# Kernel tuning notes

Hardware: AMD Instinct MI355X
Metric: run time of the kernel (lower is better)

The kernel has to match this reference:

```python
import jax, jax.numpy as jnp
import numpy as np

N_HEAD = 16
RMS_EPS = 1.1920928955078125e-07  # torch F.rms_norm default eps = finfo(fp32).eps


def _rope_tables(seq_len, head_dim, dtype):
    steps = jnp.arange(seq_len, dtype=jnp.float32)
    rates = 10000.0 ** (-jnp.arange(0, head_dim, 2, dtype=jnp.float32) / head_dim)
    angles = jnp.outer(steps, rates)  # [S, D/2]
    return jnp.cos(angles).astype(dtype)[None, None], jnp.sin(angles).astype(dtype)[None, None]


def _apply_rotary(x, cos, sin):
    # interleaved RoPE: pairs (x[2i], x[2i+1]) rotated
    left = x[..., ::2]
    right = x[..., 1::2]
    lo = left * cos - right * sin
    ro = left * sin + right * cos
    return jnp.stack((lo, ro), axis=-1).reshape(x.shape)


def _rms_norm(x, eps=RMS_EPS):
    ms = jnp.mean(jnp.square(x), axis=-1, keepdims=True)
    return x * jax.lax.rsqrt(ms + eps)


def setup_inputs() -> dict:
    key = jax.random.key(0)
    k1, k2, k3 = jax.random.split(key, 3)
    B, S, E = 2, 2048, 2048
    x = jax.random.normal(k1, (B, S, E), dtype=jnp.float32)
    w_qkv = jax.random.normal(k2, (3 * E, E), dtype=jnp.float32) * (E ** -0.5)
    w_proj = jax.random.normal(k3, (E, E), dtype=jnp.float32) * (E ** -0.5)
    return {"x": x, "w_qkv": w_qkv, "w_proj": w_proj}


def reference(x, w_qkv, w_proj):
    B, S, E = x.shape
    H = N_HEAD
    D = E // H

    qkv = x @ w_qkv.T  # [B, S, 3E]
    q, k, v = jnp.split(qkv, 3, axis=-1)
    # [B, S, E] -> [B, H, S, D]
    q = q.reshape(B, S, H, D).transpose(0, 2, 1, 3)
    k = k.reshape(B, S, H, D).transpose(0, 2, 1, 3)
    v = v.reshape(B, S, H, D).transpose(0, 2, 1, 3)

    cos, sin = _rope_tables(S, D, x.dtype)  # [1,1,S,D/2]
    q = _apply_rotary(q, cos, sin)
    k = _apply_rotary(k, cos, sin)

    q = _rms_norm(q)
    k = _rms_norm(k)

    scale = 1.0 / jnp.sqrt(jnp.asarray(D, dtype=x.dtype))
    scores = jnp.einsum("bhqd,bhkd->bhqk", q, k) * scale  # [B,H,S,S]
    causal = jnp.tril(jnp.ones((S, S), dtype=bool))
    scores = jnp.where(causal[None, None], scores, jnp.asarray(-jnp.inf, dtype=scores.dtype))
    attn = jax.nn.softmax(scores, axis=-1)
    y = jnp.einsum("bhqk,bhkd->bhqd", attn, v)  # [B,H,S,D]
    y = y.transpose(0, 2, 1, 3).reshape(B, S, E)
    return y @ w_proj.T
```

## Files before the change

### kernel.cpp

```cpp
#include <hip/hip_runtime.h>

typedef unsigned short ushort_t;
using bf16x8 = __attribute__((ext_vector_type(8))) short;
using f32x4  = __attribute__((ext_vector_type(4))) float;

#define DEV static __device__ __forceinline__

DEV unsigned short f2bf(float f) {
  union { float f; unsigned u; } a; a.f = f;
  unsigned r = a.u + 0x7fffu + ((a.u >> 16) & 1u);
  return (unsigned short)(r >> 16);
}
DEV float bf2f(unsigned short u) {
  union { unsigned u; float f; } a; a.u = ((unsigned)u) << 16;
  return a.f;
}
DEV void load_lds16(const void* g, void* l) {
  __builtin_amdgcn_global_load_lds(
      (const __attribute__((address_space(1))) void*)g,
      (__attribute__((address_space(3))) void*)l, 16, 0, 0);
}

__global__ __launch_bounds__(256) void cast_kernel(
    const float* __restrict__ src, ushort_t* __restrict__ dst, int n4) {
  int i = blockIdx.x * 256 + threadIdx.x;
  if (i >= n4) return;
  float4 f = ((const float4*)src)[i];
  ushort4 o;
  o.x = f2bf(f.x); o.y = f2bf(f.y); o.z = f2bf(f.z); o.w = f2bf(f.w);
  ((ushort4*)dst)[i] = o;
}

__global__ __launch_bounds__(256) void rope_tables_kernel(float* __restrict__ tab) {
  int idx = blockIdx.x * 256 + threadIdx.x;
  int s = idx >> 6, i = idx & 63;
  float rate = exp2f(-13.287712379549449f * ((float)(2 * i) * (1.0f / 128.0f)));
  float ang = (float)s * rate;
  tab[idx * 2]     = cosf(ang);
  tab[idx * 2 + 1] = sinf(ang);
}

template<int BM, int BN, int OUTF32>
__global__ __launch_bounds__(256, 2) void gemm_bal(
    const ushort_t* __restrict__ A, const ushort_t* __restrict__ Bm,
    void* __restrict__ C, int M, int N, int K) {
  constexpr int MF   = BM / 32;
  constexpr int NF   = BN / 32;
  constexpr int NCA  = BM / 64;
  constexpr int NCB  = BN / 64;
  constexpr int NC   = NCA + NCB;
  constexpr int ABY  = BM * 64;
  constexpr int BUFB = (BM + BN) * 64;
  __shared__ __align__(16) char lds[2 * BUFB];

  const int nby = M / BM;
  const int nwg = nby * (N / BN);
  const int orig = blockIdx.x;
  const int wgid = (orig & 7) * (nwg >> 3) + (orig >> 3);
  const int bm = (wgid % nby) * BM;
  const int bn = (wgid / nby) * BN;

  const int tid = threadIdx.x;
  const int lane = tid & 63;
  const int wave = tid >> 6;
  const int ql = lane & 15, lk = lane >> 4;
  const int wm = wave >> 1, wn = wave & 1;

  f32x4 acc[MF][NF];
#pragma unroll
  for (int m = 0; m < MF; ++m)
#pragma unroll
    for (int n = 0; n < NF; ++n) acc[m][n] = (f32x4){0.f, 0.f, 0.f, 0.f};

  const int rin  = tid >> 2;
  const int sswz = ((tid & 3) ^ ((rin >> 1) & 3)) * 16;
  const size_t rb = (size_t)K * 2;
  const char* src[NC];
#pragma unroll
  for (int c = 0; c < NCA; ++c)
    src[c] = (const char*)A + (size_t)(bm + c * 64 + rin) * rb + sswz;
#pragma unroll
  for (int c = 0; c < NCB; ++c)
    src[NCA + c] = (const char*)Bm + (size_t)(bn + c * 64 + rin) * rb + sswz;
  char* const ldsc = (char*)lds;
  const int dT = tid * 16;

  int aOff[MF], bOff[NF];
#pragma unroll
  for (int m = 0; m < MF; ++m) {
    const int r = wm * (BM / 2) + m * 16 + ql;
    aOff[m] = r * 64 + ((lk ^ ((r >> 1) & 3)) * 16);
  }
#pragma unroll
  for (int n = 0; n < NF; ++n) {
    const int r = wn * (BN / 2) + n * 16 + ql;
    bOff[n] = ABY + r * 64 + ((lk ^ ((r >> 1) & 3)) * 16);
  }

#define STAGE(BB, KT) do {                                   \
    char* d_ = ldsc + (BB) * BUFB + dT;                      \
    const size_t ko_ = (size_t)(KT) * 64;                    \
    _Pragma("unroll")                                        \
    for (int c = 0; c < NC; ++c)                             \
      load_lds16(src[c] + ko_, d_ + c * 4096);               \
  } while (0)
#define MFMA(a, b, c) __builtin_amdgcn_mfma_f32_16x16x32_bf16(a, b, c, 0, 0, 0)

  const int ns = K >> 5;
  STAGE(0, 0);
  __syncthreads();

  for (int t = 0; t < ns; ++t) {
    const int nk = (t + 1 < ns) ? t + 1 : t;
    STAGE((t + 1) & 1, nk);
    const char* sb = ldsc + (t & 1) * BUFB;
    bf16x8 bF[NF], aF[MF];
#pragma unroll
    for (int n = 0; n < NF; ++n) bF[n] = *(const bf16x8*)(sb + bOff[n]);
#pragma unroll
    for (int m = 0; m < MF; ++m) aF[m] = *(const bf16x8*)(sb + aOff[m]);
    __builtin_amdgcn_s_setprio(1);
#pragma unroll
    for (int m = 0; m < MF; ++m)
#pragma unroll
      for (int n = 0; n < NF; ++n)
        acc[m][n] = MFMA(aF[m], bF[n], acc[m][n]);
    __builtin_amdgcn_s_setprio(0);
    __syncthreads();
  }
#undef STAGE
#undef MFMA

#pragma unroll
  for (int m = 0; m < MF; ++m)
#pragma unroll
    for (int i = 0; i < 4; ++i) {
      const size_t row = (size_t)(bm + wm * (BM / 2) + m * 16 + lk * 4 + i);
#pragma unroll
      for (int n = 0; n < NF; ++n) {
        const size_t col = (size_t)(bn + wn * (BN / 2) + n * 16 + ql);
        float v = acc[m][n][i];
        if (OUTF32) ((float*)C)[row * (size_t)N + col] = v;
        else        ((ushort_t*)C)[row * (size_t)N + col] = f2bf(v);
      }
    }
}

__global__ __launch_bounds__(256) void rope_rms_kernel(
    const ushort_t* __restrict__ qkv, ushort_t* __restrict__ q,
    ushort_t* __restrict__ k, ushort_t* __restrict__ vt,
    const float* __restrict__ tab) {
  const int lane = threadIdx.x & 63;
  const int row  = blockIdx.x * 4 + (threadIdx.x >> 6);
  const int h = row & 15;
  int t = row >> 4;
  const int which = t % 3; t /= 3;
  const int s = t & 2047;
  const int b = t >> 11;
  const size_t src = ((size_t)(b * 2048 + s)) * 6144 + which * 2048 + h * 128 + lane * 2;
  ushort2 xv = *(const ushort2*)&qkv[src];
  if (which == 2) {
    size_t vbase = ((size_t)((b * 16 + h) * 128 + lane * 2)) * 2048 + s;
    vt[vbase]        = xv.x;
    vt[vbase + 2048] = xv.y;
    return;
  }
  float lo = bf2f(xv.x), ro = bf2f(xv.y);
  const float2 cs = *(const float2*)&tab[(s * 64 + lane) * 2];
  float l2 = lo * cs.x - ro * cs.y;
  float r2 = lo * cs.y + ro * cs.x;
  float ss = l2 * l2 + r2 * r2;
#pragma unroll
  for (int off = 1; off < 64; off <<= 1) ss += __shfl_xor(ss, off);
  float inv = rsqrtf(ss * (1.0f / 128.0f) + 1.1920928955078125e-07f);
  if (which == 0) inv *= 0.1275174398f;
  lo = l2 * inv; ro = r2 * inv;
  ushort_t* dst = (which == 0) ? q : k;
  ushort2 o; o.x = f2bf(lo); o.y = f2bf(ro);
  *(ushort2*)&dst[(((size_t)(b * 16 + h)) * 2048 + s) * 128 + lane * 2] = o;
}

__global__ __launch_bounds__(256, 1) void attn_kernel(
    const ushort_t* __restrict__ Q, const ushort_t* __restrict__ K,
    const ushort_t* __restrict__ VT, ushort_t* __restrict__ Y) {
  __shared__ __align__(16) ushort_t sK[2][64 * 128];
  __shared__ __align__(16) ushort_t sV[2][128 * 64];
  const int bh = blockIdx.x;
  const int yp = blockIdx.y;
  const int wave = threadIdx.x >> 6, lane = threadIdx.x & 63;
  const int ql = lane & 15, lk = lane >> 4;
  const size_t hq = (size_t)bh * 2048 * 128;
  const int b = bh >> 4, h = bh & 15;

  const char* kB = (const char*)(K + hq);
  const char* vB = (const char*)(VT + hq);
  const char* kSrc[4]; char* kDst[4];
  const char* vSrc[4]; char* vDst[4];
#pragma unroll
  for (int t = 0; t < 4; ++t) {
    int r = wave * 16 + t * 4 + (lane >> 4);
    int kgr = r >> 4, lkr = (r >> 2) & 3, ir = r & 3;
    int rho = (kgr >> 1) * 32 + lkr * 8 + (kgr & 1) * 4 + ir;
    kSrc[t] = kB + rho * 256 + (((lane & 15) * 16) ^ ((r & 7) << 4));
    kDst[t] = (char*)sK + (wave * 256 + t * 64 + lane) * 16;
    int d = wave * 32 + t * 8 + (lane >> 3);
    vSrc[t] = vB + (size_t)d * 4096 + (((lane & 7) * 16) ^ ((d & 7) << 4));
    vDst[t] = (char*)sV + (wave * 256 + t * 64 + lane) * 16;
  }

#define STAGEKV(KT, BB) do {                                         \
    _Pragma("unroll")                                                \
    for (int t_ = 0; t_ < 4; ++t_) {                                 \
      load_lds16(kSrc[t_] + (size_t)(KT) * 16384, kDst[t_] + (BB) * 16384); \
      load_lds16(vSrc[t_] + (KT) * 128, vDst[t_] + (BB) * 16384);    \
    }                                                                \
  } while (0)

  int buf = 0;
  STAGEKV(0, 0);
  __syncthreads();

  for (int pass = 0; pass < 2; ++pass) {
    const int qt = pass ? (15 - yp) : yp;
    const int ktmax = 2 * qt + 1;
    const int q0 = qt * 128 + wave * 32 + ql;

    bf16x8 qf[2][4];
#pragma unroll
    for (int g = 0; g < 2; ++g)
#pragma unroll
      for (int ks = 0; ks < 4; ++ks)
        qf[g][ks] = *(const bf16x8*)&Q[hq + (size_t)(q0 + g * 16) * 128 + ks * 32 + lk * 8];

    f32x4 acc[2][8];
#pragma unroll
    for (int g = 0; g < 2; ++g)
#pragma unroll
      for (int dg = 0; dg < 8; ++dg) acc[g][dg] = (f32x4){0.f, 0.f, 0.f, 0.f};
    float mrow[2] = {-3.0e38f, -3.0e38f}, lsum[2] = {0.f, 0.f};

    for (int kt = 0; kt <= ktmax; ++kt) {
      const int nk = (kt < ktmax) ? kt + 1 : (pass == 0 ? 0 : ktmax);
      STAGEKV(nk, buf ^ 1);
      const char* sKb = (const char*)sK + buf * 16384;
      const char* sVb = (const char*)sV + buf * 16384;

      f32x4 st[2][4];
#pragma unroll
      for (int g = 0; g < 2; ++g)
#pragma unroll
        for (int kg = 0; kg < 4; ++kg) st[g][kg] = (f32x4){0.f, 0.f, 0.f, 0.f};
#pragma unroll
      for (int kg = 0; kg < 4; ++kg) {
        const int row = kg * 16 + ql;
        const int rswz = (row & 7) << 4;
#pragma unroll
        for (int ks = 0; ks < 4; ++ks) {
          bf16x8 kf = *(const bf16x8*)(sKb + row * 256 + ((ks * 64 + lk * 16) ^ rswz));
          st[0][kg] = __builtin_amdgcn_mfma_f32_16x16x32_bf16(kf, qf[0][ks], st[0][kg], 0, 0, 0);
          st[1][kg] = __builtin_amdgcn_mfma_f32_16x16x32_bf16(kf, qf[1][ks], st[1][kg], 0, 0, 0);
        }
      }
      bf16x8 pb[2][2];
#pragma unroll
      for (int g = 0; g < 2; ++g) {
        const int q = q0 + g * 16;
        float sv[4][4]; float mp = -3.0e38f;
#pragma unroll
        for (int kg = 0; kg < 4; ++kg) {
          const int kl = ((kg >> 1) << 5) + lk * 8 + ((kg & 1) << 2);
#pragma unroll
          for (int i = 0; i < 4; ++i) {
            const int key = kt * 64 + kl + i;
            float v = (key <= q) ? st[g][kg][i] : -3.0e38f;
            sv[kg][i] = v;
            mp = fmaxf(mp, v);
          }
        }
        mp = fmaxf(mp, __shfl_xor(mp, 16));
        mp = fmaxf(mp, __shfl_xor(mp, 32));
        const float mn = fmaxf(mrow[g], mp);
        const float corr = exp2f(mrow[g] - mn);
        mrow[g] = mn;
        float p[4][4]; float rs = 0.f;
#pragma unroll
        for (int kg = 0; kg < 4; ++kg)
#pragma unroll
          for (int i = 0; i < 4; ++i) {
            float e = exp2f(sv[kg][i] - mn);
            p[kg][i] = e; rs += e;
          }
        rs += __shfl_xor(rs, 16);
        rs += __shfl_xor(rs, 32);
        lsum[g] = lsum[g] * corr + rs;
#pragma unroll
        for (int dg = 0; dg < 8; ++dg)
#pragma unroll
          for (int i = 0; i < 4; ++i) acc[g][dg][i] *= corr;
#pragma unroll
        for (int c = 0; c < 2; ++c) {
          union { bf16x8 v; ushort_t u[8]; } pk;
#pragma unroll
          for (int j = 0; j < 8; ++j) pk.u[j] = f2bf(p[2 * c + (j >> 2)][j & 3]);
          pb[g][c] = pk.v;
        }
      }
#pragma unroll
      for (int dg = 0; dg < 8; ++dg) {
        const int d = dg * 16 + ql;
        const int dswz = (d & 7) << 4;
#pragma unroll
        for (int c = 0; c < 2; ++c) {
          bf16x8 vf = *(const bf16x8*)(sVb + d * 128 + ((c * 64 + lk * 16) ^ dswz));
          acc[0][dg] = __builtin_amdgcn_mfma_f32_16x16x32_bf16(vf, pb[0][c], acc[0][dg], 0, 0, 0);
          acc[1][dg] = __builtin_amdgcn_mfma_f32_16x16x32_bf16(vf, pb[1][c], acc[1][dg], 0, 0, 0);
        }
      }
      __syncthreads();
      buf ^= 1;
    }

#pragma unroll
    for (int g = 0; g < 2; ++g) {
      const float inv = 1.0f / lsum[g];
      const size_t orow = ((size_t)(b * 2048 + q0 + g * 16)) * 2048 + h * 128;
#pragma unroll
      for (int dg = 0; dg < 8; ++dg) {
        ushort4 o;
        o.x = f2bf(acc[g][dg][0] * inv);
        o.y = f2bf(acc[g][dg][1] * inv);
        o.z = f2bf(acc[g][dg][2] * inv);
        o.w = f2bf(acc[g][dg][3] * inv);
        *(ushort4*)&Y[orow + dg * 16 + lk * 4] = o;
      }
    }
  }
#undef STAGEKV
}

extern "C" void kernel_launch(void* const* d_in, const int* in_sizes, int n_in,
                              void* d_out, int out_size, void* d_ws, size_t ws_size,
                              hipStream_t stream) {
  const float* x     = (const float*)d_in[0];
  const float* wqkv  = (const float*)d_in[1];
  const float* wproj = (const float*)d_in[2];
  float* out = (float*)d_out;
  char* ws = (char*)d_ws;

  ushort_t* x_bf     = (ushort_t*)(ws);
  ushort_t* wqkv_bf  = (ushort_t*)(ws + 16777216);
  ushort_t* wproj_bf = (ushort_t*)(ws + 41943040);
  ushort_t* qkv_bf   = (ushort_t*)(ws + 50331648);
  ushort_t* q_bf     = (ushort_t*)(ws + 100663296);
  ushort_t* k_bf     = (ushort_t*)(ws + 117440512);
  ushort_t* vt_bf    = (ushort_t*)(ws + 134217728);
  float*    tab      = (float*)(ws + 150994944);
  if (ws_size < 152043520u) return;

  cast_kernel<<<8192, 256, 0, stream>>>(x, x_bf, 2097152);
  cast_kernel<<<12288, 256, 0, stream>>>(wqkv, wqkv_bf, 3145728);
  cast_kernel<<<4096, 256, 0, stream>>>(wproj, wproj_bf, 1048576);
  rope_tables_kernel<<<512, 256, 0, stream>>>(tab);

  gemm_bal<256, 128, 0><<<768, 256, 0, stream>>>(x_bf, wqkv_bf, qkv_bf, 4096, 6144, 2048);

  rope_rms_kernel<<<49152, 256, 0, stream>>>(qkv_bf, q_bf, k_bf, vt_bf, tab);

  attn_kernel<<<dim3(32, 8), 256, 0, stream>>>(q_bf, k_bf, vt_bf, qkv_bf );

  gemm_bal<128, 128, 1><<<512, 256, 0, stream>>>(qkv_bf, wproj_bf, out, 4096, 2048, 2048);
}
```

Measured before the change: 339.8 us.

## Split attention into one block per query tile and merge cast kernels

The attention kernel previously paired two query tiles (yp and 15-yp) per block across two sequential passes over 256 blocks. It now launches 512 blocks, each handling a single query tile, ordered heaviest-first so the longer causal tiles start early. Launch bounds change to allow two blocks per CU. The three fp32-to-bf16 cast launches are also fused into one kernel that branches on the index range. This should raise parallelism and occupancy on a 256-CU part and trim launch overhead, at the cost of relying on the hardware scheduler to balance the now-uneven block sizes and possible register pressure under the tighter bound.

```diff
diff --git a/kernel.cpp b/kernel.cpp
--- a/kernel.cpp
+++ b/kernel.cpp
@@ -21,14 +21,19 @@
       (__attribute__((address_space(3))) void*)l, 16, 0, 0);
 }
 
-__global__ __launch_bounds__(256) void cast_kernel(
-    const float* __restrict__ src, ushort_t* __restrict__ dst, int n4) {
+__global__ __launch_bounds__(256) void cast3_kernel(
+    const float* __restrict__ x, const float* __restrict__ wqkv,
+    const float* __restrict__ wproj, ushort_t* __restrict__ xb,
+    ushort_t* __restrict__ qb, ushort_t* __restrict__ pb) {
   int i = blockIdx.x * 256 + threadIdx.x;
-  if (i >= n4) return;
-  float4 f = ((const float4*)src)[i];
+  const float4* s; ushort4* d; int off;
+  if (i < 2097152)      { s = (const float4*)x;     d = (ushort4*)xb; off = i; }
+  else if (i < 5242880) { s = (const float4*)wqkv;  d = (ushort4*)qb; off = i - 2097152; }
+  else                  { s = (const float4*)wproj; d = (ushort4*)pb; off = i - 5242880; }
+  float4 f = s[off];
   ushort4 o;
   o.x = f2bf(f.x); o.y = f2bf(f.y); o.z = f2bf(f.z); o.w = f2bf(f.w);
-  ((ushort4*)dst)[i] = o;
+  d[off] = o;
 }
 
 __global__ __launch_bounds__(256) void rope_tables_kernel(float* __restrict__ tab) {
@@ -180,13 +185,14 @@
   *(ushort2*)&dst[(((size_t)(b * 16 + h)) * 2048 + s) * 128 + lane * 2] = o;
 }
 
-__global__ __launch_bounds__(256, 1) void attn_kernel(
+__global__ __launch_bounds__(256, 2) void attn_kernel(
     const ushort_t* __restrict__ Q, const ushort_t* __restrict__ K,
     const ushort_t* __restrict__ VT, ushort_t* __restrict__ Y) {
   __shared__ __align__(16) ushort_t sK[2][64 * 128];
   __shared__ __align__(16) ushort_t sV[2][128 * 64];
-  const int bh = blockIdx.x;
-  const int yp = blockIdx.y;
+  const int gx = blockIdx.x;
+  const int bh = gx & 31;
+  const int qt = (gx < 256) ? (15 - (gx >> 5)) : ((gx - 256) >> 5);
   const int wave = threadIdx.x >> 6, lane = threadIdx.x & 63;
   const int ql = lane & 15, lk = lane >> 4;
   const size_t hq = (size_t)bh * 2048 * 128;
@@ -216,123 +222,120 @@
     }                                                                \
   } while (0)
 
-  int buf = 0;
+  const int ktmax = 2 * qt + 1;
+  const int q0 = qt * 128 + wave * 32 + ql;
+
+  bf16x8 qf[2][4];
+#pragma unroll
+  for (int g = 0; g < 2; ++g)
+#pragma unroll
+    for (int ks = 0; ks < 4; ++ks)
+      qf[g][ks] = *(const bf16x8*)&Q[hq + (size_t)(q0 + g * 16) * 128 + ks * 32 + lk * 8];
+
+  f32x4 acc[2][8];
+#pragma unroll
+  for (int g = 0; g < 2; ++g)
+#pragma unroll
+    for (int dg = 0; dg < 8; ++dg) acc[g][dg] = (f32x4){0.f, 0.f, 0.f, 0.f};
+  float mrow[2] = {-3.0e38f, -3.0e38f}, lsum[2] = {0.f, 0.f};
+
   STAGEKV(0, 0);
   __syncthreads();
-
-  for (int pass = 0; pass < 2; ++pass) {
-    const int qt = pass ? (15 - yp) : yp;
-    const int ktmax = 2 * qt + 1;
-    const int q0 = qt * 128 + wave * 32 + ql;
-
-    bf16x8 qf[2][4];
+  int buf = 0;
+
+  for (int kt = 0; kt <= ktmax; ++kt) {
+    const int nk = (kt < ktmax) ? kt + 1 : kt;
+    STAGEKV(nk, buf ^ 1);
+    const char* sKb = (const char*)sK + buf * 16384;
+    const char* sVb = (const char*)sV + buf * 16384;
+
+    f32x4 st[2][4];
 #pragma unroll
     for (int g = 0; g < 2; ++g)
 #pragma unroll
-      for (int ks = 0; ks < 4; ++ks)
-        qf[g][ks] = *(const bf16x8*)&Q[hq + (size_t)(q0 + g * 16) * 128 + ks * 32 + lk * 8];
-
-    f32x4 acc[2][8];
-#pragma unroll
-    for (int g = 0; g < 2; ++g)
-#pragma unroll
-      for (int dg = 0; dg < 8; ++dg) acc[g][dg] = (f32x4){0.f, 0.f, 0.f, 0.f};
-    float mrow[2] = {-3.0e38f, -3.0e38f}, lsum[2] = {0.f, 0.f};
-
-    for (int kt = 0; kt <= ktmax; ++kt) {
-      const int nk = (kt < ktmax) ? kt + 1 : (pass == 0 ? 0 : ktmax);
-      STAGEKV(nk, buf ^ 1);
-      const char* sKb = (const char*)sK + buf * 16384;
-      const char* sVb = (const char*)sV + buf * 16384;
-
-      f32x4 st[2][4];
-#pragma unroll
-      for (int g = 0; g < 2; ++g)
-#pragma unroll
-        for (int kg = 0; kg < 4; ++kg) st[g][kg] = (f32x4){0.f, 0.f, 0.f, 0.f};
+      for (int kg = 0; kg < 4; ++kg) st[g][kg] = (f32x4){0.f, 0.f, 0.f, 0.f};
+#pragma unroll
+    for (int kg = 0; kg < 4; ++kg) {
+      const int row = kg * 16 + ql;
+      const int rswz = (row & 7) << 4;
+#pragma unroll
+      for (int ks = 0; ks < 4; ++ks) {
+        bf16x8 kf = *(const bf16x8*)(sKb + row * 256 + ((ks * 64 + lk * 16) ^ rswz));
+        st[0][kg] = __builtin_amdgcn_mfma_f32_16x16x32_bf16(kf, qf[0][ks], st[0][kg], 0, 0, 0);
+        st[1][kg] = __builtin_amdgcn_mfma_f32_16x16x32_bf16(kf, qf[1][ks], st[1][kg], 0, 0, 0);
+      }
+    }
+    bf16x8 pb[2][2];
+#pragma unroll
+    for (int g = 0; g < 2; ++g) {
+      const int q = q0 + g * 16;
+      float sv[4][4]; float mp = -3.0e38f;
 #pragma unroll
       for (int kg = 0; kg < 4; ++kg) {
-        const int row = kg * 16 + ql;
-        const int rswz = (row & 7) << 4;
-#pragma unroll
-        for (int ks = 0; ks < 4; ++ks) {
-          bf16x8 kf = *(const bf16x8*)(sKb + row * 256 + ((ks * 64 + lk * 16) ^ rswz));
-          st[0][kg] = __builtin_amdgcn_mfma_f32_16x16x32_bf16(kf, qf[0][ks], st[0][kg], 0, 0, 0);
-          st[1][kg] = __builtin_amdgcn_mfma_f32_16x16x32_bf16(kf, qf[1][ks], st[1][kg], 0, 0, 0);
+        const int kl = ((kg >> 1) << 5) + lk * 8 + ((kg & 1) << 2);
+#pragma unroll
+        for (int i = 0; i < 4; ++i) {
+          const int key = kt * 64 + kl + i;
+          float v = (key <= q) ? st[g][kg][i] : -3.0e38f;
+          sv[kg][i] = v;
+          mp = fmaxf(mp, v);
         }
       }
-      bf16x8 pb[2][2];
-#pragma unroll
-      for (int g = 0; g < 2; ++g) {
-        const int q = q0 + g * 16;
-        float sv[4][4]; float mp = -3.0e38f;
-#pragma unroll
-        for (int kg = 0; kg < 4; ++kg) {
-          const int kl = ((kg >> 1) << 5) + lk * 8 + ((kg & 1) << 2);
-#pragma unroll
-          for (int i = 0; i < 4; ++i) {
-            const int key = kt * 64 + kl + i;
-            float v = (key <= q) ? st[g][kg][i] : -3.0e38f;
-            sv[kg][i] = v;
-            mp = fmaxf(mp, v);
-          }
+      mp = fmaxf(mp, __shfl_xor(mp, 16));
+      mp = fmaxf(mp, __shfl_xor(mp, 32));
+      const float mn = fmaxf(mrow[g], mp);
+      const float corr = exp2f(mrow[g] - mn);
+      mrow[g] = mn;
+      float p[4][4]; float rs = 0.f;
+#pragma unroll
+      for (int kg = 0; kg < 4; ++kg)
+#pragma unroll
+        for (int i = 0; i < 4; ++i) {
+          float e = exp2f(sv[kg][i] - mn);
+          p[kg][i] = e; rs += e;
         }
-        mp = fmaxf(mp, __shfl_xor(mp, 16));
-        mp = fmaxf(mp, __shfl_xor(mp, 32));
-        const float mn = fmaxf(mrow[g], mp);
-        const float corr = exp2f(mrow[g] - mn);
-        mrow[g] = mn;
-        float p[4][4]; float rs = 0.f;
-#pragma unroll
-        for (int kg = 0; kg < 4; ++kg)
-#pragma unroll
-          for (int i = 0; i < 4; ++i) {
-            float e = exp2f(sv[kg][i] - mn);
-            p[kg][i] = e; rs += e;
-          }
-        rs += __shfl_xor(rs, 16);
-        rs += __shfl_xor(rs, 32);
-        lsum[g] = lsum[g] * corr + rs;
-#pragma unroll
-        for (int dg = 0; dg < 8; ++dg)
-#pragma unroll
-          for (int i = 0; i < 4; ++i) acc[g][dg][i] *= corr;
-#pragma unroll
-        for (int c = 0; c < 2; ++c) {
-          union { bf16x8 v; ushort_t u[8]; } pk;
-#pragma unroll
-          for (int j = 0; j < 8; ++j) pk.u[j] = f2bf(p[2 * c + (j >> 2)][j & 3]);
-          pb[g][c] = pk.v;
-        }
-      }
-#pragma unroll
-      for (int dg = 0; dg < 8; ++dg) {
-        const int d = dg * 16 + ql;
-        const int dswz = (d & 7) << 4;
-#pragma unroll
-        for (int c = 0; c < 2; ++c) {
-          bf16x8 vf = *(const bf16x8*)(sVb + d * 128 + ((c * 64 + lk * 16) ^ dswz));
-          acc[0][dg] = __builtin_amdgcn_mfma_f32_16x16x32_bf16(vf, pb[0][c], acc[0][dg], 0, 0, 0);
-          acc[1][dg] = __builtin_amdgcn_mfma_f32_16x16x32_bf16(vf, pb[1][c], acc[1][dg], 0, 0, 0);
-        }
-      }
-      __syncthreads();
-      buf ^= 1;
-    }
-
-#pragma unroll
-    for (int g = 0; g < 2; ++g) {
-      const float inv = 1.0f / lsum[g];
-      const size_t orow = ((size_t)(b * 2048 + q0 + g * 16)) * 2048 + h * 128;
-#pragma unroll
-      for (int dg = 0; dg < 8; ++dg) {
-        ushort4 o;
-        o.x = f2bf(acc[g][dg][0] * inv);
-        o.y = f2bf(acc[g][dg][1] * inv);
-        o.z = f2bf(acc[g][dg][2] * inv);
-        o.w = f2bf(acc[g][dg][3] * inv);
-        *(ushort4*)&Y[orow + dg * 16 + lk * 4] = o;
-      }
+      rs += __shfl_xor(rs, 16);
+      rs += __shfl_xor(rs, 32);
+      lsum[g] = lsum[g] * corr + rs;
+#pragma unroll
+      for (int dg = 0; dg < 8; ++dg)
+#pragma unroll
+        for (int i = 0; i < 4; ++i) acc[g][dg][i] *= corr;
+#pragma unroll
+      for (int c = 0; c < 2; ++c) {
+        union { bf16x8 v; ushort_t u[8]; } pk;
+#pragma unroll
+        for (int j = 0; j < 8; ++j) pk.u[j] = f2bf(p[2 * c + (j >> 2)][j & 3]);
+        pb[g][c] = pk.v;
+      }
+    }
+#pragma unroll
+    for (int dg = 0; dg < 8; ++dg) {
+      const int d = dg * 16 + ql;
+      const int dswz = (d & 7) << 4;
+#pragma unroll
+      for (int c = 0; c < 2; ++c) {
+        bf16x8 vf = *(const bf16x8*)(sVb + d * 128 + ((c * 64 + lk * 16) ^ dswz));
+        acc[0][dg] = __builtin_amdgcn_mfma_f32_16x16x32_bf16(vf, pb[0][c], acc[0][dg], 0, 0, 0);
+        acc[1][dg] = __builtin_amdgcn_mfma_f32_16x16x32_bf16(vf, pb[1][c], acc[1][dg], 0, 0, 0);
+      }
+    }
+    __syncthreads();
+    buf ^= 1;
+  }
+
+#pragma unroll
+  for (int g = 0; g < 2; ++g) {
+    const float inv = 1.0f / lsum[g];
+    const size_t orow = ((size_t)(b * 2048 + q0 + g * 16)) * 2048 + h * 128;
+#pragma unroll
+    for (int dg = 0; dg < 8; ++dg) {
+      ushort4 o;
+      o.x = f2bf(acc[g][dg][0] * inv);
+      o.y = f2bf(acc[g][dg][1] * inv);
+      o.z = f2bf(acc[g][dg][2] * inv);
+      o.w = f2bf(acc[g][dg][3] * inv);
+      *(ushort4*)&Y[orow + dg * 16 + lk * 4] = o;
     }
   }
 #undef STAGEKV
@@ -357,16 +360,14 @@
   float*    tab      = (float*)(ws + 150994944);
   if (ws_size < 152043520u) return;
 
-  cast_kernel<<<8192, 256, 0, stream>>>(x, x_bf, 2097152);
-  cast_kernel<<<12288, 256, 0, stream>>>(wqkv, wqkv_bf, 3145728);
-  cast_kernel<<<4096, 256, 0, stream>>>(wproj, wproj_bf, 1048576);
+  cast3_kernel<<<24576, 256, 0, stream>>>(x, wqkv, wproj, x_bf, wqkv_bf, wproj_bf);
   rope_tables_kernel<<<512, 256, 0, stream>>>(tab);
 
   gemm_bal<256, 128, 0><<<768, 256, 0, stream>>>(x_bf, wqkv_bf, qkv_bf, 4096, 6144, 2048);
 
   rope_rms_kernel<<<49152, 256, 0, stream>>>(qkv_bf, q_bf, k_bf, vt_bf, tab);
 
-  attn_kernel<<<dim3(32, 8), 256, 0, stream>>>(q_bf, k_bf, vt_bf, qkv_bf );
+  attn_kernel<<<512, 256, 0, stream>>>(q_bf, k_bf, vt_bf, qkv_bf );
 
   gemm_bal<128, 128, 1><<<512, 256, 0, stream>>>(qkv_bf, wproj_bf, out, 4096, 2048, 2048);
 }
```

Result: faster. 329.1 us (-3.1%).
